# Kernel optimization log

Hardware: AMD Instinct MI355X
Metric: run time of the kernel (lower is better)

The kernel has to match this reference:

```python
import jax, jax.numpy as jnp
import numpy as np

B, K, D = 8, 1024, 512
H, DQ, DV = 8, 64, 64


def setup_inputs() -> dict:
    key = jax.random.key(0)
    ks = jax.random.split(key, 11)
    s = 0.02  # param init scale
    return {
        "query": jax.random.normal(ks[0], (B, K, D), jnp.float32),
        "key": jax.random.normal(ks[1], (B, K, D), jnp.float32),
        "value": jax.random.normal(ks[2], (B, K, D), jnp.float32),
        "Wq": jax.random.normal(ks[3], (D, H * DQ), jnp.float32) * s,
        "bq": jax.random.normal(ks[4], (H * DQ,), jnp.float32) * s,
        "Wk": jax.random.normal(ks[5], (D, H * DQ), jnp.float32) * s,
        "bk": jax.random.normal(ks[6], (H * DQ,), jnp.float32) * s,
        "Wv": jax.random.normal(ks[7], (D, H * DV), jnp.float32) * s,
        "bv": jax.random.normal(ks[8], (H * DV,), jnp.float32) * s,
        "Wo": jax.random.normal(ks[9], (H * DV, D), jnp.float32) * s,
        "bo": jax.random.normal(ks[10], (D,), jnp.float32) * s,
    }


def reference(query, key, value, Wq, bq, Wk, bk, Wv, bv, Wo, bo):
    b, k, _ = query.shape
    # Linear projections, split into heads: chunk(h, dim=-1) + cat(dim=0)
    # is equivalent to reshape (b, k, h, d) with head on a separate axis.
    q = (query @ Wq + bq).reshape(b, k, H, DQ)  # b k h dq
    kk = (key @ Wk + bk).reshape(b, k, H, DQ)   # b k h dq
    v = (value @ Wv + bv).reshape(b, k, H, DV)  # b k h dv
    # NOTE: original scales by sqrt(K) (sequence length), not sqrt(dq).
    scale = 1.0 / jnp.sqrt(jnp.asarray(k, q.dtype))
    scores = jnp.einsum("bqhd,bkhd->bhqk", q, kk) * scale
    attn = jax.nn.softmax(scores, axis=-1)
    ctx = jnp.einsum("bhqk,bkhd->bqhd", attn, v).reshape(b, k, H * DV)
    return ctx @ Wo + bo
```

## Files before the change

### kernel.cpp

```cpp
#include <hip/hip_runtime.h>
#include <hip/hip_bf16.h>

#define DEVI __device__ __forceinline__

typedef __attribute__((ext_vector_type(4))) float f32x4;
typedef __attribute__((ext_vector_type(8))) short bf16x8;

static constexpr int BB  = 8;
static constexpr int SEQ = 1024;
static constexpr int DIM = 512;
static constexpr int NH  = 8;
static constexpr int HD  = 64;
static constexpr int M   = BB * SEQ;


DEVI unsigned short f2bf(float x) {
  unsigned int u = __builtin_bit_cast(unsigned int, x);
  u += 0x7fffu + ((u >> 16) & 1u);
  return (unsigned short)(u >> 16);
}

DEVI float fexp2(float x) {
#if __has_builtin(__builtin_amdgcn_exp2f)
  return __builtin_amdgcn_exp2f(x);
#else
  float r; asm("v_exp_f32 %0, %1" : "=v"(r) : "v"(x)); return r;
#endif
}

DEVI void gload_lds16(const unsigned short* g, unsigned short* l) {
  __builtin_amdgcn_global_load_lds(
      (const __attribute__((address_space(1))) void*)g,
      (__attribute__((address_space(3))) void*)l, 16, 0, 0);
}


__global__ __launch_bounds__(256) void cvt3_kernel(const float* __restrict__ a,
                                                   const float* __restrict__ b,
                                                   const float* __restrict__ c,
                                                   unsigned short* __restrict__ oa,
                                                   unsigned short* __restrict__ ob,
                                                   unsigned short* __restrict__ oc) {
  const float* in = (blockIdx.y == 0) ? a : ((blockIdx.y == 1) ? b : c);
  unsigned short* out = (blockIdx.y == 0) ? oa : ((blockIdx.y == 1) ? ob : oc);
  int i = (blockIdx.x * 256 + threadIdx.x) * 4;
  float4 v = *reinterpret_cast<const float4*>(in + i);
  ushort4 o;
  o.x = f2bf(v.x); o.y = f2bf(v.y); o.z = f2bf(v.z); o.w = f2bf(v.w);
  *reinterpret_cast<ushort4*>(out + i) = o;
}


__global__ __launch_bounds__(256) void cvt_t4_kernel(const float* __restrict__ w0,
                                                     const float* __restrict__ w1,
                                                     const float* __restrict__ w2,
                                                     const float* __restrict__ w3,
                                                     unsigned short* __restrict__ o0,
                                                     unsigned short* __restrict__ o1,
                                                     unsigned short* __restrict__ o2,
                                                     unsigned short* __restrict__ o3) {
  const float* in = (blockIdx.z == 0) ? w0 : ((blockIdx.z == 1) ? w1 : ((blockIdx.z == 2) ? w2 : w3));
  unsigned short* out = (blockIdx.z == 0) ? o0 : ((blockIdx.z == 1) ? o1 : ((blockIdx.z == 2) ? o2 : o3));
  __shared__ float tile[32][33];
  int n0 = blockIdx.x * 32, k0 = blockIdx.y * 32;
  int tx = threadIdx.x & 31, ty = threadIdx.x >> 5;
#pragma unroll
  for (int r = 0; r < 32; r += 8)
    tile[ty + r][tx] = in[(size_t)(k0 + ty + r) * DIM + n0 + tx];
  __syncthreads();
#pragma unroll
  for (int r = 0; r < 32; r += 8)
    out[(size_t)(n0 + ty + r) * DIM + k0 + tx] = f2bf(tile[tx][ty + r]);
}


template <bool OUT_F32>
DEVI void gemm_body(const unsigned short* __restrict__ A,
                    const unsigned short* __restrict__ Bt,
                    const float* __restrict__ bias,
                    float gs,
                    void* __restrict__ Cout) {
  __shared__ unsigned short lA[128 * 32];
  __shared__ unsigned short lB[128 * 32];
  const int tid = threadIdx.x;
  const int lane = tid & 63, wave = tid >> 6;
  const int wr = wave >> 1, wc = wave & 1;
  const int row0 = blockIdx.x * 128, col0 = blockIdx.y * 128;
  const int lr = lane & 15, lg = lane >> 4;

  f32x4 acc[4][4] = {};

  for (int k0 = 0; k0 < DIM; k0 += 32) {
    __syncthreads();
#pragma unroll
    for (int c = 0; c < 2; ++c) {
      int s0 = c * 256 + wave * 64;
      int s = s0 + lane;
      int r = s >> 2, ko = (s & 3) * 8;
      gload_lds16(A + (size_t)(row0 + r) * DIM + k0 + ko, &lA[s0 * 8]);
      gload_lds16(Bt + (size_t)(col0 + r) * DIM + k0 + ko, &lB[s0 * 8]);
    }
    __syncthreads();
    bf16x8 af[4], bfr[4];
#pragma unroll
    for (int m = 0; m < 4; ++m)
      af[m] = *reinterpret_cast<const bf16x8*>(&lA[(wr * 64 + m * 16 + lr) * 32 + lg * 8]);
#pragma unroll
    for (int n = 0; n < 4; ++n)
      bfr[n] = *reinterpret_cast<const bf16x8*>(&lB[(wc * 64 + n * 16 + lr) * 32 + lg * 8]);
    __builtin_amdgcn_s_setprio(1);
#pragma unroll
    for (int m = 0; m < 4; ++m)
#pragma unroll
      for (int n = 0; n < 4; ++n)
        acc[m][n] = __builtin_amdgcn_mfma_f32_16x16x32_bf16(af[m], bfr[n], acc[m][n], 0, 0, 0);
    __builtin_amdgcn_s_setprio(0);
  }

#pragma unroll
  for (int m = 0; m < 4; ++m) {
#pragma unroll
    for (int n = 0; n < 4; ++n) {
      int col = col0 + wc * 64 + n * 16 + lr;
      int r0 = row0 + wr * 64 + m * 16 + lg * 4;
      float bv = bias[col];
#pragma unroll
      for (int j = 0; j < 4; ++j) {
        float val = (acc[m][n][j] + bv) * gs;
        if constexpr (OUT_F32)
          reinterpret_cast<float*>(Cout)[(size_t)(r0 + j) * DIM + col] = val;
        else
          reinterpret_cast<unsigned short*>(Cout)[(size_t)(r0 + j) * DIM + col] = f2bf(val);
      }
    }
  }
}

struct GemmArgs {
  const unsigned short* A;
  const unsigned short* Bt;
  const float* bias;
  unsigned short* C;
  float scale;
};

__global__ __launch_bounds__(256) void gemm_proj(GemmArgs a0, GemmArgs a1, GemmArgs a2) {
  GemmArgs g = (blockIdx.z == 0) ? a0 : ((blockIdx.z == 1) ? a1 : a2);
  gemm_body<false>(g.A, g.Bt, g.bias, g.scale, (void*)g.C);
}

__global__ __launch_bounds__(256) void gemm_out(const unsigned short* __restrict__ A,
                                                const unsigned short* __restrict__ Bt,
                                                const float* __restrict__ bias,
                                                float* __restrict__ C) {
  gemm_body<true>(A, Bt, bias, 1.0f, (void*)C);
}


__global__ __launch_bounds__(256) void transpose_v_kernel(const unsigned short* __restrict__ vbuf,
                                                          unsigned short* __restrict__ vT) {
  __shared__ unsigned short t[64 * 64];
  const int b = blockIdx.z, h = blockIdx.y, s0 = blockIdx.x * 64;
  const int tid = threadIdx.x, lane = tid & 63, wave = tid >> 6;

#pragma unroll
  for (int it = 0; it < 2; ++it) {
    int base = wave * 128 + it * 64;
    int idx = base + lane;
    int r = idx >> 3, c = idx & 7;
    int csrc = c ^ (r >> 3);
    gload_lds16(vbuf + ((size_t)(b * SEQ) + s0 + r) * DIM + h * HD + csrc * 8,
                &t[base * 8]);
  }
  __syncthreads();

#pragma unroll
  for (int it = 0; it < 2; ++it) {
    int o = it * 256 + tid;
    int dv = o >> 3, cs = o & 7;
    bf16x8 v;
#pragma unroll
    for (int k = 0; k < 8; ++k) {
      int s = cs * 8 + k;
      v[k] = (short)t[s * 64 + (((dv >> 3) ^ (s >> 3)) << 3) + (dv & 7)];
    }
    *reinterpret_cast<bf16x8*>(vT + ((size_t)((b * NH + h) * HD) + dv) * SEQ + s0 + cs * 8) = v;
  }
}


__global__ __launch_bounds__(512) void attn_kernel(const unsigned short* __restrict__ qb,
                                                   const unsigned short* __restrict__ kb,
                                                   const unsigned short* __restrict__ vT,
                                                   unsigned short* __restrict__ ctx) {
  __shared__ unsigned short lK[2][64 * 64];
  __shared__ unsigned short lV[2][64 * 64];
  __shared__ unsigned short Pl[8][16 * 72];

  const int b = blockIdx.z, h = blockIdx.y;
  const int tid = threadIdx.x, lane = tid & 63, wave = tid >> 6;
  const int lr = lane & 15, lg = lane >> 4;
  const int q0 = blockIdx.x * 128 + wave * 16;

  const int sr = tid >> 3, sc = (tid & 7) ^ (sr & 7);
  const unsigned short* Kbase = kb + ((size_t)b * SEQ) * DIM + (size_t)h * HD;
  const unsigned short* Vbase = vT + (size_t)(b * NH + h) * HD * SEQ;

  bf16x8 qf0, qf1;
  {
    const unsigned short* qrow = qb + ((size_t)(b * SEQ) + q0 + lr) * DIM + h * HD;
    qf0 = *reinterpret_cast<const bf16x8*>(qrow + lg * 8);
    qf1 = *reinterpret_cast<const bf16x8*>(qrow + 32 + lg * 8);
  }

  float l_r[4] = {0.f, 0.f, 0.f, 0.f};
  f32x4 o_acc[4];
#pragma unroll
  for (int n = 0; n < 4; ++n) o_acc[n] = f32x4{0.f, 0.f, 0.f, 0.f};

  unsigned short* pw = Pl[wave];

  gload_lds16(Kbase + (size_t)sr * DIM + sc * 8, &lK[0][(wave * 64) * 8]);
  gload_lds16(Vbase + (size_t)sr * SEQ + sc * 8, &lV[0][(wave * 64) * 8]);
  __syncthreads();

  for (int t = 0; t < SEQ / 64; ++t) {
    const int cur = t & 1;
    if (t + 1 < SEQ / 64) {
      const int nk = (t + 1) * 64;
      gload_lds16(Kbase + (size_t)(nk + sr) * DIM + sc * 8, &lK[cur ^ 1][(wave * 64) * 8]);
      gload_lds16(Vbase + (size_t)sr * SEQ + nk + sc * 8, &lV[cur ^ 1][(wave * 64) * 8]);
    }

    f32x4 st[4];
    __builtin_amdgcn_s_setprio(1);
#pragma unroll
    for (int kt = 0; kt < 4; ++kt) {
      const int row = kt * 16 + lr;
      const char* rbase = (const char*)&lK[cur][0] + row * 128;
      const int sw = (row & 7) << 4;
      bf16x8 kf0 = *reinterpret_cast<const bf16x8*>(rbase + ((lg * 16) ^ sw));
      bf16x8 kf1 = *reinterpret_cast<const bf16x8*>(rbase + ((64 + lg * 16) ^ sw));
      f32x4 a = {};
      a = __builtin_amdgcn_mfma_f32_16x16x32_bf16(qf0, kf0, a, 0, 0, 0);
      a = __builtin_amdgcn_mfma_f32_16x16x32_bf16(qf1, kf1, a, 0, 0, 0);
      st[kt] = a;
    }
    __builtin_amdgcn_s_setprio(0);

#pragma unroll
    for (int j = 0; j < 4; ++j) {
      float p0 = fexp2(st[0][j]);
      float p1 = fexp2(st[1][j]);
      float p2 = fexp2(st[2][j]);
      float p3 = fexp2(st[3][j]);
      l_r[j] += (p0 + p1) + (p2 + p3);
      const int qrow = (lg * 4 + j) * 72;
      pw[qrow + lr] = f2bf(p0);
      pw[qrow + 16 + lr] = f2bf(p1);
      pw[qrow + 32 + lr] = f2bf(p2);
      pw[qrow + 48 + lr] = f2bf(p3);
    }

#pragma unroll
    for (int c = 0; c < 2; ++c) {
      bf16x8 pf = *reinterpret_cast<const bf16x8*>((const char*)pw + lr * 144 + c * 64 + lg * 16);
      __builtin_amdgcn_s_setprio(1);
#pragma unroll
      for (int n = 0; n < 4; ++n) {
        const int row = n * 16 + lr;
        bf16x8 vf = *reinterpret_cast<const bf16x8*>(
            (const char*)&lV[cur][0] + row * 128 + ((c * 64 + lg * 16) ^ ((row & 7) << 4)));
        o_acc[n] = __builtin_amdgcn_mfma_f32_16x16x32_bf16(pf, vf, o_acc[n], 0, 0, 0);
      }
      __builtin_amdgcn_s_setprio(0);
    }

    __syncthreads();
  }

  float invl[4];
#pragma unroll
  for (int j = 0; j < 4; ++j) {
    float l = l_r[j];
#pragma unroll
    for (int msk = 1; msk < 16; msk <<= 1) l += __shfl_xor(l, msk);
    invl[j] = 1.f / l;
  }
#pragma unroll
  for (int n = 0; n < 4; ++n)
#pragma unroll
    for (int j = 0; j < 4; ++j)
      pw[(lg * 4 + j) * 72 + n * 16 + lr] = f2bf(o_acc[n][j] * invl[j]);

#pragma unroll
  for (int it = 0; it < 2; ++it) {
    int idx = it * 64 + lane;
    int r = idx >> 3, cc = idx & 7;
    bf16x8 v = *reinterpret_cast<const bf16x8*>((const char*)pw + r * 144 + cc * 16);
    *reinterpret_cast<bf16x8*>(ctx + ((size_t)(b * SEQ) + q0 + r) * DIM + h * HD + cc * 8) = v;
  }
}


extern "C" void kernel_launch(void* const* d_in, const int* in_sizes, int n_in,
                              void* d_out, int out_size, void* d_ws, size_t ws_size,
                              hipStream_t stream) {
  const float* query = (const float*)d_in[0];
  const float* key_  = (const float*)d_in[1];
  const float* value = (const float*)d_in[2];
  const float* Wq = (const float*)d_in[3];
  const float* bq = (const float*)d_in[4];
  const float* Wk = (const float*)d_in[5];
  const float* bk = (const float*)d_in[6];
  const float* Wv = (const float*)d_in[7];
  const float* bv = (const float*)d_in[8];
  const float* Wo = (const float*)d_in[9];
  const float* bo = (const float*)d_in[10];
  float* out = (float*)d_out;

  unsigned short* ws = (unsigned short*)d_ws;
  const size_t NM = (size_t)M * DIM;
  const size_t NW = (size_t)DIM * DIM;
  unsigned short* xq   = ws;
  unsigned short* xk   = xq + NM;
  unsigned short* xv   = xk + NM;
  unsigned short* qb   = xv + NM;
  unsigned short* kbuf = qb + NM;
  unsigned short* vbuf = kbuf + NM;
  unsigned short* ctx  = vbuf + NM;
  unsigned short* Wqt  = ctx + NM;
  unsigned short* Wkt  = Wqt + NW;
  unsigned short* Wvt  = Wkt + NW;
  unsigned short* Wot  = Wvt + NW;
  unsigned short* vTb  = xq;

  cvt3_kernel<<<dim3((int)(NM / 1024), 3), 256, 0, stream>>>(query, key_, value, xq, xk, xv);
  cvt_t4_kernel<<<dim3(16, 16, 4), 256, 0, stream>>>(Wq, Wk, Wv, Wo, Wqt, Wkt, Wvt, Wot);

  const float qscale = 0.03125f * 1.4426950408889634f;
  GemmArgs g0{xq, Wqt, bq, qb, qscale}, g1{xk, Wkt, bk, kbuf, 1.0f}, g2{xv, Wvt, bv, vbuf, 1.0f};
  gemm_proj<<<dim3(M / 128, DIM / 128, 3), 256, 0, stream>>>(g0, g1, g2);

  transpose_v_kernel<<<dim3(SEQ / 64, NH, BB), 256, 0, stream>>>(vbuf, vTb);

  attn_kernel<<<dim3(SEQ / 128, NH, BB), 512, 0, stream>>>(qb, kbuf, vTb, ctx);

  gemm_out<<<dim3(M / 128, DIM / 128), 256, 0, stream>>>(ctx, Wot, bo, out);
}
```

Baseline: 88.14 us.

## Double-buffer LDS tiles in projection GEMM to overlap loads with MFMA

Turns the GEMM's shared-memory A/B tiles into two buffers. The next K-slice is prefetched into the alternate buffer while MFMAs run on the current one, and one barrier per iteration replaces two. This aims to hide global-to-LDS load latency behind compute, at the cost of doubling LDS use, which may lower occupancy. It also relies on the direct-to-LDS loads having completed by the time the barrier is reached.

```diff
diff --git a/kernel.cpp b/kernel.cpp
--- a/kernel.cpp
+++ b/kernel.cpp
@@ -80,8 +80,8 @@
                     const float* __restrict__ bias,
                     float gs,
                     void* __restrict__ Cout) {
-  __shared__ unsigned short lA[128 * 32];
-  __shared__ unsigned short lB[128 * 32];
+  __shared__ unsigned short lA[2][128 * 32];
+  __shared__ unsigned short lB[2][128 * 32];
   const int tid = threadIdx.x;
   const int lane = tid & 63, wave = tid >> 6;
   const int wr = wave >> 1, wc = wave & 1;
@@ -90,24 +90,34 @@
 
   f32x4 acc[4][4] = {};
 
-  for (int k0 = 0; k0 < DIM; k0 += 32) {
-    __syncthreads();
-#pragma unroll
-    for (int c = 0; c < 2; ++c) {
-      int s0 = c * 256 + wave * 64;
-      int s = s0 + lane;
-      int r = s >> 2, ko = (s & 3) * 8;
-      gload_lds16(A + (size_t)(row0 + r) * DIM + k0 + ko, &lA[s0 * 8]);
-      gload_lds16(Bt + (size_t)(col0 + r) * DIM + k0 + ko, &lB[s0 * 8]);
-    }
-    __syncthreads();
+  const int s0a = wave * 64;
+  const int sA = s0a + lane, rA = sA >> 2, koA = (sA & 3) * 8;
+  const int s0b = 256 + wave * 64;
+  const int sB = s0b + lane, rB = sB >> 2, koB = (sB & 3) * 8;
+
+#define GEMM_STAGE(buf, k0)                                                        \
+  do {                                                                             \
+    gload_lds16(A + (size_t)(row0 + rA) * DIM + (k0) + koA, &lA[buf][s0a * 8]);    \
+    gload_lds16(Bt + (size_t)(col0 + rA) * DIM + (k0) + koA, &lB[buf][s0a * 8]);   \
+    gload_lds16(A + (size_t)(row0 + rB) * DIM + (k0) + koB, &lA[buf][s0b * 8]);    \
+    gload_lds16(Bt + (size_t)(col0 + rB) * DIM + (k0) + koB, &lB[buf][s0b * 8]);   \
+  } while (0)
+
+  GEMM_STAGE(0, 0);
+  __syncthreads();
+
+  constexpr int NT = DIM / 32;
+  for (int t = 0; t < NT; ++t) {
+    const int cur = t & 1;
+    if (t + 1 < NT) GEMM_STAGE(cur ^ 1, (t + 1) * 32);
+
     bf16x8 af[4], bfr[4];
 #pragma unroll
     for (int m = 0; m < 4; ++m)
-      af[m] = *reinterpret_cast<const bf16x8*>(&lA[(wr * 64 + m * 16 + lr) * 32 + lg * 8]);
+      af[m] = *reinterpret_cast<const bf16x8*>(&lA[cur][(wr * 64 + m * 16 + lr) * 32 + lg * 8]);
 #pragma unroll
     for (int n = 0; n < 4; ++n)
-      bfr[n] = *reinterpret_cast<const bf16x8*>(&lB[(wc * 64 + n * 16 + lr) * 32 + lg * 8]);
+      bfr[n] = *reinterpret_cast<const bf16x8*>(&lB[cur][(wc * 64 + n * 16 + lr) * 32 + lg * 8]);
     __builtin_amdgcn_s_setprio(1);
 #pragma unroll
     for (int m = 0; m < 4; ++m)
@@ -115,7 +125,10 @@
       for (int n = 0; n < 4; ++n)
         acc[m][n] = __builtin_amdgcn_mfma_f32_16x16x32_bf16(af[m], bfr[n], acc[m][n], 0, 0, 0);
     __builtin_amdgcn_s_setprio(0);
-  }
+
+    __syncthreads();
+  }
+#undef GEMM_STAGE
 
 #pragma unroll
   for (int m = 0; m < 4; ++m) {
```

New measurement: 87.44 us. Within noise of the previous version (-0.8%).
